# Kernel optimization log

Hardware: AMD Instinct MI355X
Metric: run time of the kernel (lower is better)

The kernel has to match this reference:

```python
import jax, jax.numpy as jnp
import numpy as np

N_NODES = 50000
N_EDGES = 800000
IN_DIM = 128
HEADS = 4
HID = 32
NEG_SLOPE = 0.2


def setup_inputs() -> dict:
    key = jax.random.key(0)
    ks = jax.random.split(key, 10)

    def glorot(k, shape, fan):
        return jax.random.normal(k, shape, jnp.float32) * (1.0 / np.sqrt(fan))

    x = jax.random.normal(ks[0], (N_NODES, IN_DIM), jnp.float32)
    edge_index = jax.random.randint(ks[1], (2, N_EDGES), 0, N_NODES)
    # layer 1: in=IN_DIM, out=HEADS*HID (concat)
    Wl1 = glorot(ks[2], (IN_DIM, HEADS * HID), IN_DIM)
    Wr1 = glorot(ks[3], (IN_DIM, HEADS * HID), IN_DIM)
    att1 = glorot(ks[4], (HEADS, HID), HID)
    b1 = jnp.zeros((HEADS * HID,), jnp.float32)
    # layer 2: in=HEADS*HID, out=HID (mean over heads)
    Wl2 = glorot(ks[5], (HEADS * HID, HEADS * HID), HEADS * HID)
    Wr2 = glorot(ks[6], (HEADS * HID, HEADS * HID), HEADS * HID)
    att2 = glorot(ks[7], (HEADS, HID), HID)
    b2 = jnp.zeros((HID,), jnp.float32)
    return {"x": x, "edge_index": edge_index, "Wl1": Wl1, "Wr1": Wr1,
            "att1": att1, "b1": b1, "Wl2": Wl2, "Wr2": Wr2,
            "att2": att2, "b2": b2}


def _gatv2_conv(x, src, dst, Wl, Wr, att, bias, concat):
    """PyG GATv2Conv (eval mode, self loops already in src/dst)."""
    n = x.shape[0]
    h, c = att.shape
    xl = (x @ Wl).reshape(n, h, c)  # source transform
    xr = (x @ Wr).reshape(n, h, c)  # destination transform
    e = jax.nn.leaky_relu(xl[src] + xr[dst], NEG_SLOPE)   # [E, H, C]
    logits = jnp.einsum('ehc,hc->eh', e, att)             # [E, H]
    # segment softmax over edges grouped by destination node
    m = jax.ops.segment_max(logits, dst, num_segments=n)  # [N, H]
    a = jnp.exp(logits - m[dst])
    denom = jax.ops.segment_sum(a, dst, num_segments=n)   # [N, H]
    alpha = a / denom[dst]                                # [E, H]
    out = jax.ops.segment_sum(xl[src] * alpha[..., None], dst,
                              num_segments=n)             # [N, H, C]
    out = out.reshape(n, h * c) if concat else out.mean(axis=1)
    return out + bias


def reference(x, edge_index, Wl1, Wr1, att1, b1, Wl2, Wr2, att2, b2):
    n = x.shape[0]
    loop = jnp.arange(n, dtype=edge_index.dtype)
    src = jnp.concatenate([edge_index[0], loop])
    dst = jnp.concatenate([edge_index[1], loop])
    h1 = jax.nn.relu(_gatv2_conv(x, src, dst, Wl1, Wr1, att1, b1, concat=True))
    h2 = jax.nn.relu(_gatv2_conv(h1, src, dst, Wl2, Wr2, att2, b2, concat=False))
    return h2
```

## Files before the change

### kernel.cpp

```cpp
#include <hip/hip_runtime.h>
#include <hip/hip_bf16.h>
#include <hip/hip_fp16.h>

#define HEADS 4
#define HID 32
#define DIM 128
#define CAP 64

typedef __attribute__((ext_vector_type(8))) short bf16x8;
typedef __attribute__((ext_vector_type(4))) float f32x4;

__device__ __forceinline__ float bf2f(unsigned short u) {
    return __uint_as_float(((unsigned int)u) << 16);
}
__device__ __forceinline__ unsigned short f2bf(float f) {
    unsigned int u = __float_as_uint(f);
    unsigned int r = u + 0x7fffu + ((u >> 16) & 1u);
    return (unsigned short)(r >> 16);
}
__device__ __forceinline__ float dload(const float* f, const unsigned short* b, int isb, size_t i) {
    return isb ? bf2f(b[i]) : f[i];
}
__device__ __forceinline__ float2 h2f2(unsigned int u) {
    __half2 h = *(__half2*)&u;
    return make_float2(__low2float(h), __high2float(h));
}

__global__ void detect_dtype(const unsigned short* __restrict__ xu, int* __restrict__ flag)
{
    int tid = threadIdx.x;
    float v = bf2f(xu[tid * 2]);
    float av = fabsf(v);
    int sane = (v == v && av > 1e-4f && av < 1e4f) ? 1 : 0;
    __shared__ int cnt;
    if (tid == 0) cnt = 0;
    __syncthreads();
    atomicAdd(&cnt, sane);
    __syncthreads();
    if (tid == 0) *flag = (cnt >= 128) ? 1 : 0;
}

__global__ void zero_i(int* __restrict__ p, int n)
{
    int i = blockIdx.x * blockDim.x + threadIdx.x;
    if (i < n) p[i] = 0;
}

__global__ void scatter_edges(const int* __restrict__ ei, int E,
                              int* __restrict__ cnt, int* __restrict__ bucket)
{
    int e = blockIdx.x * blockDim.x + threadIdx.x;
    if (e < E) {
        int s = ei[e], d = ei[E + e];
        int slot = atomicAdd(&cnt[d], 1);
        if (slot < CAP) bucket[(size_t)d * CAP + slot] = s;
    }
}

__global__ void wprep(const float* __restrict__ Wlf, const unsigned short* __restrict__ Wlb,
                      const float* __restrict__ Wrf, const unsigned short* __restrict__ Wrb,
                      const int* __restrict__ flag, uint4* __restrict__ wf)
{
    const int gtid = blockIdx.x * blockDim.x + threadIdx.x;
    if (gtid >= 16 * 4 * 64) return;
    const int isb = *flag;
    const int lane = gtid & 63;
    const int ks = (gtid >> 6) & 3;
    const int nt = gtid >> 8;
    const int col = nt * 16 + (lane & 15);
    const int kbase = ks * 32 + (lane >> 4) * 8;
    unsigned short hs[8], ls[8];
#pragma unroll
    for (int j = 0; j < 8; ++j) {
        int k = kbase + j;
        float w = (col < 128) ? dload(Wlf, Wlb, isb, (size_t)k * 128 + col)
                              : dload(Wrf, Wrb, isb, (size_t)k * 128 + col - 128);
        hs[j] = f2bf(w);
        ls[j] = f2bf(w - bf2f(hs[j]));
    }
    uint4 H, L;
    H.x = hs[0] | ((unsigned)hs[1] << 16); H.y = hs[2] | ((unsigned)hs[3] << 16);
    H.z = hs[4] | ((unsigned)hs[5] << 16); H.w = hs[6] | ((unsigned)hs[7] << 16);
    L.x = ls[0] | ((unsigned)ls[1] << 16); L.y = ls[2] | ((unsigned)ls[3] << 16);
    L.z = ls[4] | ((unsigned)ls[5] << 16); L.w = ls[6] | ((unsigned)ls[7] << 16);
    wf[((0 * 16 + nt) * 4 + ks) * 64 + lane] = H;
    wf[((1 * 16 + nt) * 4 + ks) * 64 + lane] = L;
}

template<bool X_DUAL>
__global__ void __launch_bounds__(256, 2)
mfma_gemm(const float* __restrict__ xf, const unsigned short* __restrict__ xb,
          const uint4* __restrict__ wf, const int* __restrict__ flag,
          unsigned short* __restrict__ xlh, float* __restrict__ xr, int N)
{
    const int isb = *flag;
    const int tid = threadIdx.x;
    const int base = blockIdx.x * 64;
    __shared__ uint4 ldsA[2 * 4 * 4 * 64];

#pragma unroll
    for (int it = 0; it < 4; ++it) {
        int t = tid + it * 256;
        int r = t >> 4, kb = t & 15;
        int row = base + r;
        float v[8];
        if (row < N) {
            size_t idx = (size_t)row * DIM + kb * 8;
            if (X_DUAL && isb) {
#pragma unroll
                for (int j = 0; j < 8; ++j) v[j] = bf2f(xb[idx + j]);
            } else {
                float4 p0 = *(const float4*)(xf + idx);
                float4 p1 = *(const float4*)(xf + idx + 4);
                v[0] = p0.x; v[1] = p0.y; v[2] = p0.z; v[3] = p0.w;
                v[4] = p1.x; v[5] = p1.y; v[6] = p1.z; v[7] = p1.w;
            }
        } else {
#pragma unroll
            for (int j = 0; j < 8; ++j) v[j] = 0.f;
        }
        unsigned short hs[8], ls[8];
#pragma unroll
        for (int j = 0; j < 8; ++j) {
            hs[j] = f2bf(v[j]);
            ls[j] = f2bf(v[j] - bf2f(hs[j]));
        }
        uint4 H, L;
        H.x = hs[0] | ((unsigned)hs[1] << 16); H.y = hs[2] | ((unsigned)hs[3] << 16);
        H.z = hs[4] | ((unsigned)hs[5] << 16); H.w = hs[6] | ((unsigned)hs[7] << 16);
        L.x = ls[0] | ((unsigned)ls[1] << 16); L.y = ls[2] | ((unsigned)ls[3] << 16);
        L.z = ls[4] | ((unsigned)ls[5] << 16); L.w = ls[6] | ((unsigned)ls[7] << 16);
        int mtile = r >> 4, kstep = kb >> 2, lane = (kb & 3) * 16 + (r & 15);
        ldsA[((0 * 4 + mtile) * 4 + kstep) * 64 + lane] = H;
        ldsA[((1 * 4 + mtile) * 4 + kstep) * 64 + lane] = L;
    }
    __syncthreads();

    const int w = tid >> 6, lane = tid & 63;
    const int nloc = lane & 15;
    const int e0 = (lane >> 4) << 2;

#pragma unroll 2
    for (int ntq = 0; ntq < 4; ++ntq) {
        const int nt = w * 4 + ntq;
        bf16x8 bh[4], bl[4];
#pragma unroll
        for (int ks = 0; ks < 4; ++ks) {
            bh[ks] = *(const bf16x8*)&wf[((0 * 16 + nt) * 4 + ks) * 64 + lane];
            bl[ks] = *(const bf16x8*)&wf[((1 * 16 + nt) * 4 + ks) * 64 + lane];
        }
#pragma unroll
        for (int mt = 0; mt < 4; ++mt) {
            f32x4 a0 = {0.f, 0.f, 0.f, 0.f};
            f32x4 a1 = {0.f, 0.f, 0.f, 0.f};
            f32x4 a2 = {0.f, 0.f, 0.f, 0.f};
#pragma unroll
            for (int ks = 0; ks < 4; ++ks) {
                bf16x8 ah = *(bf16x8*)&ldsA[((0 * 4 + mt) * 4 + ks) * 64 + lane];
                bf16x8 al = *(bf16x8*)&ldsA[((1 * 4 + mt) * 4 + ks) * 64 + lane];
                a0 = __builtin_amdgcn_mfma_f32_16x16x32_bf16(ah, bh[ks], a0, 0, 0, 0);
                a1 = __builtin_amdgcn_mfma_f32_16x16x32_bf16(al, bh[ks], a1, 0, 0, 0);
                a2 = __builtin_amdgcn_mfma_f32_16x16x32_bf16(ah, bl[ks], a2, 0, 0, 0);
            }
            f32x4 acc = a0 + a1 + a2;
            const int r0 = base + mt * 16 + e0;
            if (nt < 8) {
                const int col = nt * 16 + nloc;
#pragma unroll
                for (int e = 0; e < 4; ++e) {
                    int row = r0 + e;
                    if (row < N) xlh[(size_t)row * DIM + col] = __half_as_ushort(__float2half(acc[e]));
                }
            } else {
                const int col = nt * 16 + nloc - 128;
#pragma unroll
                for (int e = 0; e < 4; ++e) {
                    int row = r0 + e;
                    if (row < N) xr[(size_t)row * DIM + col] = acc[e];
                }
            }
        }
    }
}

template<int LAYER>
__global__ void fused_node(const unsigned short* __restrict__ xlh, const float* __restrict__ xr,
                           const int* __restrict__ bucket, const int* __restrict__ cnt,
                           const float* __restrict__ attf, const unsigned short* __restrict__ attb,
                           const float* __restrict__ bf_, const unsigned short* __restrict__ bb,
                           const int* __restrict__ flag, int N, void* __restrict__ outp)
{
    const int node = blockIdx.x * 4 + (threadIdx.x >> 6);
    if (node >= N) return;
    const int l = threadIdx.x & 63;
    const int isb = *flag;
    const unsigned int* xl2 = (const unsigned int*)xlh;

    const float att0 = dload(attf, attb, isb, 2 * l);
    const float att1 = dload(attf, attb, isb, 2 * l + 1);
    const float2 rv = *(const float2*)(xr + (size_t)node * DIM + 2 * l);

    int deg = cnt[node];
    deg = deg < CAP ? deg : CAP;
    const int m = deg + 1;
    const int* bk = bucket + (size_t)node * CAP;

    const int myslot = (l < deg) ? bk[l] : node;
#define SRCOF(J) ((J) < deg ? __shfl(myslot, (J) & 63) : node)

    unsigned int b[4];
#pragma unroll
    for (int p = 0; p < 4; ++p) b[p] = xl2[(size_t)SRCOF(p) * 64 + l];

    float num0 = 0.f, num1 = 0.f, den = 0.f;
    for (int j = 0; j < m; j += 4) {
#pragma unroll
        for (int p = 0; p < 4; ++p) {
            float2 v = h2f2(b[p]);
            b[p] = xl2[(size_t)SRCOF(j + 4 + p) * 64 + l];
            float u0 = v.x + rv.x, u1 = v.y + rv.y;
            float t = fmaf(att0, fmaf(0.2f, fminf(u0, 0.f), fmaxf(u0, 0.f)),
                           att1 * fmaf(0.2f, fminf(u1, 0.f), fmaxf(u1, 0.f)));
#pragma unroll
            for (int off = 1; off < 16; off <<= 1) t += __shfl_xor(t, off);
            float a = (j + p < m) ? __expf(fminf(fmaxf(t, -50.f), 50.f)) : 0.f;
            den += a;
            num0 = fmaf(a, v.x, num0);
            num1 = fmaf(a, v.y, num1);
        }
    }
#undef SRCOF
    float o0 = num0 / den, o1 = num1 / den;

    if (LAYER == 1) {
        float w0 = o0 + dload(bf_, bb, isb, 2 * l);
        float w1 = o1 + dload(bf_, bb, isb, 2 * l + 1);
        float2 st = make_float2(w0 > 0.f ? w0 : 0.f, w1 > 0.f ? w1 : 0.f);
        *(float2*)((float*)outp + (size_t)node * DIM + 2 * l) = st;
    } else {
        float s0v = o0, s1v = o1;
        s0v += __shfl_xor(s0v, 16); s0v += __shfl_xor(s0v, 32);
        s1v += __shfl_xor(s1v, 16); s1v += __shfl_xor(s1v, 32);
        if (l < 16) {
            float v0 = 0.25f * s0v + dload(bf_, bb, isb, 2 * l);
            float v1 = 0.25f * s1v + dload(bf_, bb, isb, 2 * l + 1);
            v0 = v0 > 0.f ? v0 : 0.f;
            v1 = v1 > 0.f ? v1 : 0.f;
            if (isb) {
                unsigned int pk = (unsigned int)f2bf(v0) | ((unsigned int)f2bf(v1) << 16);
                *(unsigned int*)((unsigned short*)outp + (size_t)node * HID + 2 * l) = pk;
            } else {
                *(float2*)((float*)outp + (size_t)node * HID + 2 * l) = make_float2(v0, v1);
            }
        }
    }
}

extern "C" void kernel_launch(void* const* d_in, const int* in_sizes, int n_in,
                              void* d_out, int out_size, void* d_ws, size_t ws_size,
                              hipStream_t stream)
{
#define DUAL(i) (const float*)d_in[i], (const unsigned short*)d_in[i]
    const int* ei = (const int*)d_in[1];

    const int N = in_sizes[0] / DIM;
    const int E = in_sizes[1] / 2;

    float* ws = (float*)d_ws;
    const size_t NF = (size_t)N * DIM;
    unsigned short* f_xlh = (unsigned short*)ws;
    float* f_xr   = ws + NF / 2;
    float* f_h1   = f_xr + NF;
    int*   bucket = (int*)(f_h1 + NF);
    int*   cnt    = bucket + (size_t)N * CAP;
    int*   flag   = cnt + N;
    size_t wf_off = ((size_t)(flag + 1) - (size_t)d_ws + 15) & ~(size_t)15;
    uint4* wfrag1 = (uint4*)((char*)d_ws + wf_off);
    uint4* wfrag2 = wfrag1 + 8192;

    const dim3 B(256);
    const int gemm_blocks = (N + 63) / 64;
    const int node_blocks = (N + 3) / 4;

    detect_dtype<<<1, B, 0, stream>>>((const unsigned short*)d_in[0], flag);

    zero_i<<<(N + 255) / 256, B, 0, stream>>>(cnt, N);
    scatter_edges<<<(E + 255) / 256, B, 0, stream>>>(ei, E, cnt, bucket);
    wprep<<<16, B, 0, stream>>>(DUAL(2), DUAL(3), flag, wfrag1);
    wprep<<<16, B, 0, stream>>>(DUAL(6), DUAL(7), flag, wfrag2);

    mfma_gemm<true><<<gemm_blocks, B, 0, stream>>>(DUAL(0), wfrag1, flag, f_xlh, f_xr, N);
    fused_node<1><<<node_blocks, B, 0, stream>>>(f_xlh, f_xr, bucket, cnt, DUAL(4), DUAL(5),
                                                 flag, N, f_h1);

    mfma_gemm<false><<<gemm_blocks, B, 0, stream>>>(f_h1, nullptr, wfrag2, flag, f_xlh, f_xr, N);
    fused_node<2><<<node_blocks, B, 0, stream>>>(f_xlh, f_xr, bucket, cnt, DUAL(8), DUAL(9),
                                                 flag, N, d_out);
#undef DUAL
}
```

Before: 301.7 us.

## Merge prep kernels, raise GEMM occupancy, split softmax loop tail

Folds the counter-zeroing and both weight-fragment preparation kernels into a single prep launch, removing two kernel launches. Raises the GEMM launch-bounds occupancy hint from 2 to 4 blocks and disables unrolling of the n-tile loop, which lowers register pressure at the cost of less instruction-level parallelism. Splits the per-node aggregation loop into full groups of four without per-element bounds checks plus a guarded remainder, so the main loop no longer predicates the exp.

```diff
diff --git a/kernel.cpp b/kernel.cpp
--- a/kernel.cpp
+++ b/kernel.cpp
@@ -40,30 +40,12 @@
     if (tid == 0) *flag = (cnt >= 128) ? 1 : 0;
 }
 
-__global__ void zero_i(int* __restrict__ p, int n)
-{
-    int i = blockIdx.x * blockDim.x + threadIdx.x;
-    if (i < n) p[i] = 0;
-}
-
-__global__ void scatter_edges(const int* __restrict__ ei, int E,
-                              int* __restrict__ cnt, int* __restrict__ bucket)
-{
-    int e = blockIdx.x * blockDim.x + threadIdx.x;
-    if (e < E) {
-        int s = ei[e], d = ei[E + e];
-        int slot = atomicAdd(&cnt[d], 1);
-        if (slot < CAP) bucket[(size_t)d * CAP + slot] = s;
-    }
-}
-
-__global__ void wprep(const float* __restrict__ Wlf, const unsigned short* __restrict__ Wlb,
+__device__ __forceinline__ void wprep_block(int blk,
+                      const float* __restrict__ Wlf, const unsigned short* __restrict__ Wlb,
                       const float* __restrict__ Wrf, const unsigned short* __restrict__ Wrb,
-                      const int* __restrict__ flag, uint4* __restrict__ wf)
-{
-    const int gtid = blockIdx.x * blockDim.x + threadIdx.x;
-    if (gtid >= 16 * 4 * 64) return;
-    const int isb = *flag;
+                      int isb, uint4* __restrict__ wf)
+{
+    const int gtid = blk * 256 + threadIdx.x;
     const int lane = gtid & 63;
     const int ks = (gtid >> 6) & 3;
     const int nt = gtid >> 8;
@@ -87,8 +69,37 @@
     wf[((1 * 16 + nt) * 4 + ks) * 64 + lane] = L;
 }
 
+__global__ void prep(int* __restrict__ cnt, int N, int ZB, const int* __restrict__ flag,
+                     const float* Wl1f, const unsigned short* Wl1b,
+                     const float* Wr1f, const unsigned short* Wr1b, uint4* __restrict__ wf1,
+                     const float* Wl2f, const unsigned short* Wl2b,
+                     const float* Wr2f, const unsigned short* Wr2b, uint4* __restrict__ wf2)
+{
+    int b = blockIdx.x;
+    if (b < ZB) {
+        int i = b * 256 + threadIdx.x;
+        if (i < N) cnt[i] = 0;
+        return;
+    }
+    const int isb = *flag;
+    b -= ZB;
+    if (b < 16) wprep_block(b, Wl1f, Wl1b, Wr1f, Wr1b, isb, wf1);
+    else        wprep_block(b - 16, Wl2f, Wl2b, Wr2f, Wr2b, isb, wf2);
+}
+
+__global__ void scatter_edges(const int* __restrict__ ei, int E,
+                              int* __restrict__ cnt, int* __restrict__ bucket)
+{
+    int e = blockIdx.x * blockDim.x + threadIdx.x;
+    if (e < E) {
+        int s = ei[e], d = ei[E + e];
+        int slot = atomicAdd(&cnt[d], 1);
+        if (slot < CAP) bucket[(size_t)d * CAP + slot] = s;
+    }
+}
+
 template<bool X_DUAL>
-__global__ void __launch_bounds__(256, 2)
+__global__ void __launch_bounds__(256, 4)
 mfma_gemm(const float* __restrict__ xf, const unsigned short* __restrict__ xb,
           const uint4* __restrict__ wf, const int* __restrict__ flag,
           unsigned short* __restrict__ xlh, float* __restrict__ xr, int N)
@@ -140,7 +151,7 @@
     const int nloc = lane & 15;
     const int e0 = (lane >> 4) << 2;
 
-#pragma unroll 2
+#pragma unroll 1
     for (int ntq = 0; ntq < 4; ++ntq) {
         const int nt = w * 4 + ntq;
         bf16x8 bh[4], bl[4];
@@ -213,7 +224,8 @@
     for (int p = 0; p < 4; ++p) b[p] = xl2[(size_t)SRCOF(p) * 64 + l];
 
     float num0 = 0.f, num1 = 0.f, den = 0.f;
-    for (int j = 0; j < m; j += 4) {
+    const int mfull = m & ~3;
+    for (int j = 0; j < mfull; j += 4) {
 #pragma unroll
         for (int p = 0; p < 4; ++p) {
             float2 v = h2f2(b[p]);
@@ -223,10 +235,28 @@
                            att1 * fmaf(0.2f, fminf(u1, 0.f), fmaxf(u1, 0.f)));
 #pragma unroll
             for (int off = 1; off < 16; off <<= 1) t += __shfl_xor(t, off);
-            float a = (j + p < m) ? __expf(fminf(fmaxf(t, -50.f), 50.f)) : 0.f;
+            float a = __expf(fminf(fmaxf(t, -50.f), 50.f));
             den += a;
             num0 = fmaf(a, v.x, num0);
             num1 = fmaf(a, v.y, num1);
+        }
+    }
+    const int rem = m - mfull;
+    if (rem) {
+#pragma unroll
+        for (int p = 0; p < 4; ++p) {
+            if (p < rem) {
+                float2 v = h2f2(b[p]);
+                float u0 = v.x + rv.x, u1 = v.y + rv.y;
+                float t = fmaf(att0, fmaf(0.2f, fminf(u0, 0.f), fmaxf(u0, 0.f)),
+                               att1 * fmaf(0.2f, fminf(u1, 0.f), fmaxf(u1, 0.f)));
+#pragma unroll
+                for (int off = 1; off < 16; off <<= 1) t += __shfl_xor(t, off);
+                float a = __expf(fminf(fmaxf(t, -50.f), 50.f));
+                den += a;
+                num0 = fmaf(a, v.x, num0);
+                num1 = fmaf(a, v.y, num1);
+            }
         }
     }
 #undef SRCOF
@@ -281,13 +311,14 @@
     const dim3 B(256);
     const int gemm_blocks = (N + 63) / 64;
     const int node_blocks = (N + 3) / 4;
+    const int ZB = (N + 255) / 256;
 
     detect_dtype<<<1, B, 0, stream>>>((const unsigned short*)d_in[0], flag);
 
-    zero_i<<<(N + 255) / 256, B, 0, stream>>>(cnt, N);
+    prep<<<ZB + 32, B, 0, stream>>>(cnt, N, ZB, flag,
+                                    DUAL(2), DUAL(3), wfrag1,
+                                    DUAL(6), DUAL(7), wfrag2);
     scatter_edges<<<(E + 255) / 256, B, 0, stream>>>(ei, E, cnt, bucket);
-    wprep<<<16, B, 0, stream>>>(DUAL(2), DUAL(3), flag, wfrag1);
-    wprep<<<16, B, 0, stream>>>(DUAL(6), DUAL(7), flag, wfrag2);
 
     mfma_gemm<true><<<gemm_blocks, B, 0, stream>>>(DUAL(0), wfrag1, flag, f_xlh, f_xr, N);
     fused_node<1><<<node_blocks, B, 0, stream>>>(f_xlh, f_xr, bucket, cnt, DUAL(4), DUAL(5),
```

Measured after the change: 377.4 us. 25.1% more time.
